# Kernel tuning notes

Measured on AMD Instinct MI355X. Metric: run time of the kernel, lower is better.

Reference implementation:

```python
import jax, jax.numpy as jnp
import numpy as np

B, T, D, H, O = 16384, 64, 64, 256, 1


def setup_inputs() -> dict:
    key = jax.random.key(0)
    ks = jax.random.split(key, 16)
    s = 0.05
    inp = {
        "x": jax.random.normal(ks[0], (B, T, D), dtype=jnp.float32),
        # RNNCell layer1: h1 = tanh(x @ W_ih1.T + b_ih1 + h1 @ W_hh1.T + b_hh1)
        "W_ih1": jax.random.normal(ks[1], (H, D), dtype=jnp.float32) * s,
        "b_ih1": jax.random.normal(ks[2], (H,), dtype=jnp.float32) * s,
        "W_hh1": jax.random.normal(ks[3], (H, H), dtype=jnp.float32) * s,
        "b_hh1": jax.random.normal(ks[4], (H,), dtype=jnp.float32) * s,
        # RNNCell layer2 (input is h1, size H)
        "W_ih2": jax.random.normal(ks[5], (H, H), dtype=jnp.float32) * s,
        "b_ih2": jax.random.normal(ks[6], (H,), dtype=jnp.float32) * s,
        "W_hh2": jax.random.normal(ks[7], (H, H), dtype=jnp.float32) * s,
        "b_hh2": jax.random.normal(ks[8], (H,), dtype=jnp.float32) * s,
        # output heads
        "W_o1": jax.random.normal(ks[9], (O, H), dtype=jnp.float32) * s,
        "b_o1": jax.random.normal(ks[10], (O,), dtype=jnp.float32) * s,
        "W_o2": jax.random.normal(ks[11], (O, H), dtype=jnp.float32) * s,
        "b_o2": jax.random.normal(ks[12], (O,), dtype=jnp.float32) * s,
        # gate: Linear(2H, H)
        "W_g": jax.random.normal(ks[13], (H, 2 * H), dtype=jnp.float32) * s,
        "b_g": jax.random.normal(ks[14], (H,), dtype=jnp.float32) * s,
    }
    return inp


def _gated_rnn(x, W_ih1, b_ih1, W_hh1, b_hh1, W_ih2, b_ih2, W_hh2, b_hh2,
               W_o1, b_o1, W_o2, b_o2, W_g, b_g):
    b = x.shape[0]
    h1_0 = jnp.zeros((b, H), dtype=x.dtype)
    h2_0 = jnp.zeros((b, H), dtype=x.dtype)
    u_0 = jnp.ones((b, H), dtype=x.dtype)

    # Precompute input projections for all timesteps: [T, B, H]
    x_proj = jnp.einsum('btd,hd->tbh', x, W_ih1) + b_ih1

    def step(carry, xp_t):
        h1, h2, u = carry
        h1 = jnp.tanh(xp_t + h1 @ W_hh1.T + b_hh1)
        z2 = jnp.tanh(h1 @ W_ih2.T + b_ih2 + h2 @ W_hh2.T + b_hh2)
        h2 = u * z2 + (1.0 - u) * h2
        out = jnp.tanh(h1 @ W_o1.T + b_o1) + jnp.tanh(h2 @ W_o2.T + b_o2)
        u = jax.nn.sigmoid(jnp.concatenate([h1, h2], axis=1) @ W_g.T + b_g)
        return (h1, h2, u), out

    _, outs = jax.lax.scan(step, (h1_0, h2_0, u_0), x_proj)  # outs: [T, B, O]
    outs = jnp.transpose(outs, (1, 0, 2))  # [B, T, O]
    if outs.shape[2] == 1:
        outs = outs[:, :, 0]  # mirror .squeeze(2)
    return outs


def reference(x, W_ih1, b_ih1, W_hh1, b_hh1, W_ih2, b_ih2, W_hh2, b_hh2,
              W_o1, b_o1, W_o2, b_o2, W_g, b_g):
    return _gated_rnn(x, W_ih1, b_ih1, W_hh1, b_hh1, W_ih2, b_ih2, W_hh2,
                      b_hh2, W_o1, b_o1, W_o2, b_o2, W_g, b_g)
```

## Files before the change

kernel.cpp:

```cpp
#include <hip/hip_runtime.h>
#include <hip/hip_bf16.h>

typedef __bf16 bf16_t;
typedef __bf16 bf16x8 __attribute__((ext_vector_type(8)));
typedef float f32x4 __attribute__((ext_vector_type(4)));
typedef int i32x4 __attribute__((ext_vector_type(4)));

#define HDIM 256
#define TSTEPS 64
#define DIN 64
#define BM 64
#define NBLK 256

__device__ __forceinline__ float fast_tanh(float x) {
    float e = __builtin_amdgcn_exp2f(x * 2.8853900817779268f);
    return 1.0f - 2.0f * __builtin_amdgcn_rcpf(e + 1.0f);
}
__device__ __forceinline__ float fast_sigmoid(float x) {
    float e = __builtin_amdgcn_exp2f(-x * 1.4426950408889634f);
    return __builtin_amdgcn_rcpf(1.0f + e);
}

__device__ __forceinline__ unsigned lds_addr(int row, int kb) {
    return (unsigned)(row * 512 + (kb ^ ((row & 7) << 4)));
}
__device__ __forceinline__ unsigned lx_addr(int row, int kb) {
    return (unsigned)(row * 128 + (kb ^ ((row & 7) << 4)));
}

__device__ __forceinline__ bf16x8 lds_ld8(const char* p) {
    return *(const bf16x8*)p;
}
__device__ __forceinline__ void lds_st1(char* p, bf16_t v) {
    *(bf16_t*)p = v;
}

#define BAR()                                                       \
    do {                                                            \
        __builtin_amdgcn_sched_barrier(0);                          \
        asm volatile("s_waitcnt lgkmcnt(0)\n\ts_barrier" ::: "memory"); \
        __builtin_amdgcn_sched_barrier(0);                          \
    } while (0)

__global__ void pack_w(const float* __restrict__ s0, const float* __restrict__ s1,
                       int ksplit, int stride0, int stride1, int off0, int off1,
                       int KC, bf16_t* __restrict__ dst) {
    int idx = blockIdx.x * 256 + threadIdx.x;
    int total = 256 * KC * 32;
    if (idx >= total) return;
    int i = idx & 7;
    int lane = (idx >> 3) & 63;
    int chunk = idx >> 9;
    int n2 = chunk & 1;
    int rest = chunk >> 1;
    int kc = rest % KC, wv = rest / KC;
    int nt = wv * 2 + n2;
    int n = nt * 16 + (lane & 15);
    int k = kc * 32 + ((lane >> 4) * 8) + i;
    float v = (k < ksplit) ? s0[n * stride0 + off0 + k]
                           : s1[n * stride1 + off1 + (k - ksplit)];
    dst[idx] = (bf16_t)v;
}

__global__ void pack_bias(const float* __restrict__ b_ih1, const float* __restrict__ b_hh1,
                          const float* __restrict__ b_ih2, const float* __restrict__ b_hh2,
                          const float* __restrict__ b_g,
                          float* __restrict__ bias1, float* __restrict__ bias2a,
                          float* __restrict__ biasg) {
    int j = threadIdx.x;
    bias1[j] = b_ih1[j] + b_hh1[j];
    bias2a[j] = b_ih2[j] + b_hh2[j];
    biasg[j] = b_g[j];
}

#define ISSUE(BUF, PB, N)                                            \
    _Pragma("unroll") for (int c = 0; c < (N); ++c)                  \
        BUF[c] = *(const bf16x8*)((PB) + c * 512 + (lane << 3));

#define GEMM_PH(NKK, BUF, ASRC, KC0, ACC)                                             \
    _Pragma("unroll") for (int kk = 0; kk < (NKK); ++kk) {                            \
        bf16x8 a_[4];                                                                 \
        _Pragma("unroll") for (int mt = 0; mt < 4; ++mt)                              \
            a_[mt] = lds_ld8((ASRC) + lds_addr(mt * 16 + l15,                         \
                                               ((KC0) + kk) * 64 + l4 * 16));         \
        _Pragma("unroll") for (int mt = 0; mt < 4; ++mt) {                            \
            ACC[mt][0] = __builtin_amdgcn_mfma_f32_16x16x32_bf16(a_[mt], BUF[kk * 2 + 0], ACC[mt][0], 0, 0, 0); \
            ACC[mt][1] = __builtin_amdgcn_mfma_f32_16x16x32_bf16(a_[mt], BUF[kk * 2 + 1], ACC[mt][1], 0, 0, 0); \
        }                                                                             \
    }

__global__ __launch_bounds__(512, 1) void rnn_main(
    const float* __restrict__ x,
    const bf16_t* __restrict__ pw_ih1,
    const bf16_t* __restrict__ pw_hh1,
    const bf16_t* __restrict__ pw_2a,
    const bf16_t* __restrict__ pw_2b,
    const bf16_t* __restrict__ pw_3,
    const float* __restrict__ bias1v, const float* __restrict__ bias2av,
    const float* __restrict__ biasgv,
    const float* __restrict__ wo1, const float* __restrict__ bo1p,
    const float* __restrict__ wo2, const float* __restrict__ bo2p,
    unsigned* __restrict__ gsync,
    float* __restrict__ out) {
    __shared__ char lds[90112];
    char* lh1 = lds;
    char* lh2 = lds + 32768;
    char* lx  = lds + 65536;
    float* lout = (float*)(lds + 73728);

    const int tid = threadIdx.x;
    const int wave = tid >> 6, lane = tid & 63;
    const int l15 = lane & 15, l4 = lane >> 4;
    const int b0 = blockIdx.x * BM;
    unsigned* gc = gsync + (blockIdx.x & 7) * 32;

    {
        i32x4 z = {0, 0, 0, 0};
        for (int i = tid; i < 4096; i += 512) ((i32x4*)lds)[i] = z;
    }

    f32x4 u_reg[4][2];
#pragma unroll
    for (int mt = 0; mt < 4; ++mt)
#pragma unroll
        for (int n2 = 0; n2 < 2; ++n2) u_reg[mt][n2] = (f32x4){1.f, 1.f, 1.f, 1.f};

    float bias1_r[2], bias2a_r[2], biasg_r[2];
#pragma unroll
    for (int n2 = 0; n2 < 2; ++n2) {
        int col = wave * 32 + n2 * 16 + l15;
        bias1_r[n2] = bias1v[col];
        bias2a_r[n2] = bias2av[col];
        biasg_r[n2] = biasgv[col];
    }
    const float bo1 = bo1p[0], bo2 = bo2p[0];
    const int orow = tid >> 3, oseg = tid & 7;
    const int xrow = tid >> 3, xc16 = (tid & 7) * 16;
    const float* xbase = x + (size_t)(b0 + xrow) * (TSTEPS * DIN) + (tid & 7) * 8;

    const bf16_t* base_ih1 = pw_ih1 + wave * 2048;
    const bf16_t* base_hh1 = pw_hh1 + wave * 8192;
    const bf16_t* base_2a  = pw_2a  + wave * 16384;
    const bf16_t* base_2b  = pw_2b  + wave * 8192;
    const bf16_t* base_3   = pw_3   + wave * 8192;

    bf16x8 R0[8], R1[8], R2[8];

    {
        f32x4 xv0 = __builtin_nontemporal_load((const f32x4*)xbase);
        f32x4 xv1 = __builtin_nontemporal_load((const f32x4*)(xbase + 4));
        bf16x8 xa;
        xa[0] = (bf16_t)xv0[0]; xa[1] = (bf16_t)xv0[1]; xa[2] = (bf16_t)xv0[2]; xa[3] = (bf16_t)xv0[3];
        xa[4] = (bf16_t)xv1[0]; xa[5] = (bf16_t)xv1[1]; xa[6] = (bf16_t)xv1[2]; xa[7] = (bf16_t)xv1[3];
        *(bf16x8*)(lx + lx_addr(xrow, xc16)) = xa;
    }
    ISSUE(R0, base_ih1, 4);
    ISSUE(R1, base_hh1, 8);
    ISSUE(R2, base_hh1 + 4096, 8);
    BAR();

    for (int t = 0; t < TSTEPS; ++t) {
        f32x4 acc[4][2];
#pragma unroll
        for (int mt = 0; mt < 4; ++mt)
#pragma unroll
            for (int n2 = 0; n2 < 2; ++n2) acc[mt][n2] = (f32x4){0.f, 0.f, 0.f, 0.f};
#pragma unroll
        for (int kk = 0; kk < 2; ++kk) {
            bf16x8 a_[4];
#pragma unroll
            for (int mt = 0; mt < 4; ++mt)
                a_[mt] = lds_ld8(lx + lx_addr(mt * 16 + l15, kk * 64 + l4 * 16));
#pragma unroll
            for (int mt = 0; mt < 4; ++mt) {
                acc[mt][0] = __builtin_amdgcn_mfma_f32_16x16x32_bf16(a_[mt], R0[kk * 2 + 0], acc[mt][0], 0, 0, 0);
                acc[mt][1] = __builtin_amdgcn_mfma_f32_16x16x32_bf16(a_[mt], R0[kk * 2 + 1], acc[mt][1], 0, 0, 0);
            }
        }
        ISSUE(R0, base_2a, 8);
        f32x4 xv0, xv1;
        {
            int tn = t + 1; if (tn > TSTEPS - 1) tn = TSTEPS - 1;
            const float* xp = xbase + tn * DIN;
            xv0 = __builtin_nontemporal_load((const f32x4*)xp);
            xv1 = __builtin_nontemporal_load((const f32x4*)(xp + 4));
        }
        GEMM_PH(4, R1, lh1, 0, acc)
        ISSUE(R1, base_2a + 4096, 8);
        GEMM_PH(4, R2, lh1, 4, acc)
        ISSUE(R2, base_2a + 8192, 8);

        float h1n[4][2][4];
#pragma unroll
        for (int mt = 0; mt < 4; ++mt)
#pragma unroll
            for (int n2 = 0; n2 < 2; ++n2)
#pragma unroll
                for (int r = 0; r < 4; ++r)
                    h1n[mt][n2][r] = fast_tanh(acc[mt][n2][r] + bias1_r[n2]);
        BAR();
#pragma unroll
        for (int mt = 0; mt < 4; ++mt)
#pragma unroll
            for (int n2 = 0; n2 < 2; ++n2)
#pragma unroll
                for (int r = 0; r < 4; ++r)
                    lds_st1(lh1 + lds_addr(mt * 16 + l4 * 4 + r,
                                           (wave * 32 + n2 * 16 + l15) * 2), (bf16_t)h1n[mt][n2][r]);
        BAR();

        f32x4 accz[4][2];
#pragma unroll
        for (int mt = 0; mt < 4; ++mt)
#pragma unroll
            for (int n2 = 0; n2 < 2; ++n2) accz[mt][n2] = (f32x4){0.f, 0.f, 0.f, 0.f};
        GEMM_PH(4, R0, lh1, 0, accz)
        ISSUE(R0, base_2a + 12288, 8);
        GEMM_PH(4, R1, lh1, 4, accz)
        ISSUE(R1, base_2b, 8);
        GEMM_PH(4, R2, lh2, 0, accz)
        ISSUE(R2, base_2b + 4096, 8);
        GEMM_PH(4, R0, lh2, 4, accz)
        ISSUE(R0, base_3, 8);

        float h2n[4][2][4];
#pragma unroll
        for (int mt = 0; mt < 4; ++mt)
#pragma unroll
            for (int n2 = 0; n2 < 2; ++n2)
#pragma unroll
                for (int r = 0; r < 4; ++r) {
                    float z2 = fast_tanh(accz[mt][n2][r] + bias2a_r[n2]);
                    float h2o = (float)*(const bf16_t*)(lh2 + lds_addr(mt * 16 + l4 * 4 + r,
                                                                       (wave * 32 + n2 * 16 + l15) * 2));
                    float un = u_reg[mt][n2][r];
                    h2n[mt][n2][r] = un * z2 + (1.f - un) * h2o;
                }
        BAR();
#pragma unroll
        for (int mt = 0; mt < 4; ++mt)
#pragma unroll
            for (int n2 = 0; n2 < 2; ++n2)
#pragma unroll
                for (int r = 0; r < 4; ++r)
                    lds_st1(lh2 + lds_addr(mt * 16 + l4 * 4 + r,
                                           (wave * 32 + n2 * 16 + l15) * 2), (bf16_t)h2n[mt][n2][r]);
        {
            bf16x8 xa;
            xa[0] = (bf16_t)xv0[0]; xa[1] = (bf16_t)xv0[1]; xa[2] = (bf16_t)xv0[2]; xa[3] = (bf16_t)xv0[3];
            xa[4] = (bf16_t)xv1[0]; xa[5] = (bf16_t)xv1[1]; xa[6] = (bf16_t)xv1[2]; xa[7] = (bf16_t)xv1[3];
            *(bf16x8*)(lx + lx_addr(xrow, xc16)) = xa;
        }

        f32x4 accg[4][2];
#pragma unroll
        for (int mt = 0; mt < 4; ++mt)
#pragma unroll
            for (int n2 = 0; n2 < 2; ++n2) accg[mt][n2] = (f32x4){0.f, 0.f, 0.f, 0.f};
        GEMM_PH(4, R1, lh1, 0, accg)
        ISSUE(R1, base_3 + 4096, 4);
        BAR();

        if (tid == 0)
            __hip_atomic_fetch_add(gc, 1u, __ATOMIC_RELAXED, __HIP_MEMORY_SCOPE_AGENT);

        GEMM_PH(4, R2, lh1, 4, accg)
        ISSUE(R2, base_3 + 6144, 4);
        GEMM_PH(4, R0, lh2, 0, accg)
        ISSUE(R0, base_ih1, 4);
        GEMM_PH(2, R1, lh2, 4, accg)
        ISSUE(R1, base_hh1, 8);
        GEMM_PH(2, R2, lh2, 6, accg)
        ISSUE(R2, base_hh1 + 4096, 8);

#pragma unroll
        for (int mt = 0; mt < 4; ++mt)
#pragma unroll
            for (int n2 = 0; n2 < 2; ++n2)
#pragma unroll
                for (int r = 0; r < 4; ++r)
                    u_reg[mt][n2][r] = fast_sigmoid(accg[mt][n2][r] + biasg_r[n2]);

        float s1 = 0.f, s2 = 0.f;
#pragma unroll
        for (int c = 0; c < 4; ++c) {
            int kb = oseg * 64 + c * 16;
            bf16x8 hv1 = lds_ld8(lh1 + lds_addr(orow, kb));
            bf16x8 hv2 = lds_ld8(lh2 + lds_addr(orow, kb));
            const float* w1p = wo1 + oseg * 32 + c * 8;
            const float* w2p = wo2 + oseg * 32 + c * 8;
            float4 w10 = *(const float4*)w1p, w11 = *(const float4*)(w1p + 4);
            float4 w20 = *(const float4*)w2p, w21 = *(const float4*)(w2p + 4);
            s1 += (float)hv1[0] * w10.x + (float)hv1[1] * w10.y + (float)hv1[2] * w10.z + (float)hv1[3] * w10.w;
            s1 += (float)hv1[4] * w11.x + (float)hv1[5] * w11.y + (float)hv1[6] * w11.z + (float)hv1[7] * w11.w;
            s2 += (float)hv2[0] * w20.x + (float)hv2[1] * w20.y + (float)hv2[2] * w20.z + (float)hv2[3] * w20.w;
            s2 += (float)hv2[4] * w21.x + (float)hv2[5] * w21.y + (float)hv2[6] * w21.z + (float)hv2[7] * w21.w;
        }
        s1 += __shfl_xor(s1, 1, 8); s1 += __shfl_xor(s1, 2, 8); s1 += __shfl_xor(s1, 4, 8);
        s2 += __shfl_xor(s2, 1, 8); s2 += __shfl_xor(s2, 2, 8); s2 += __shfl_xor(s2, 4, 8);
        if (oseg == 0)
            lout[orow * TSTEPS + t] = fast_tanh(s1 + bo1) + fast_tanh(s2 + bo2);

        if (tid == 0) {
            unsigned target = 32u * (unsigned)(t + 1);
            int guard = 0;
            while (__hip_atomic_load(gc, __ATOMIC_RELAXED, __HIP_MEMORY_SCOPE_AGENT) < target
                   && guard < 1500) {
                ++guard;
                __builtin_amdgcn_s_sleep(2);
            }
        }
        BAR();
    }

    {
        const float* lp = lout + tid * 8;
        f32x4 o0 = {lp[0], lp[1], lp[2], lp[3]};
        f32x4 o1 = {lp[4], lp[5], lp[6], lp[7]};
        float* op = out + (size_t)b0 * TSTEPS + tid * 8;
        *(f32x4*)op = o0;
        *(f32x4*)(op + 4) = o1;
    }
}

extern "C" void kernel_launch(void* const* d_in, const int* in_sizes, int n_in,
                              void* d_out, int out_size, void* d_ws, size_t ws_size,
                              hipStream_t stream) {
    const float* x = (const float*)d_in[0];
    const float* W_ih1 = (const float*)d_in[1];
    const float* b_ih1 = (const float*)d_in[2];
    const float* W_hh1 = (const float*)d_in[3];
    const float* b_hh1 = (const float*)d_in[4];
    const float* W_ih2 = (const float*)d_in[5];
    const float* b_ih2 = (const float*)d_in[6];
    const float* W_hh2 = (const float*)d_in[7];
    const float* b_hh2 = (const float*)d_in[8];
    const float* W_o1 = (const float*)d_in[9];
    const float* b_o1 = (const float*)d_in[10];
    const float* W_o2 = (const float*)d_in[11];
    const float* b_o2 = (const float*)d_in[12];
    const float* W_g = (const float*)d_in[13];
    const float* b_g = (const float*)d_in[14];

    char* ws = (char*)d_ws;
    bf16_t* pw_ih1 = (bf16_t*)(ws + 0);
    bf16_t* pw_hh1 = (bf16_t*)(ws + 32768);
    bf16_t* pw_2a = (bf16_t*)(ws + 163840);
    bf16_t* pw_2b = (bf16_t*)(ws + 425984);
    bf16_t* pw_3 = (bf16_t*)(ws + 557056);
    float* bias1 = (float*)(ws + 688128);
    float* bias2a = (float*)(ws + 689152);
    float* biasg = (float*)(ws + 690176);
    unsigned* gsync = (unsigned*)(ws + 692224);

    pack_w<<<32 * 2, 256, 0, stream>>>(W_ih1, W_ih1, 64, 64, 64, 0, 0, 2, pw_ih1);
    pack_w<<<32 * 8, 256, 0, stream>>>(W_hh1, W_hh1, 256, 256, 256, 0, 0, 8, pw_hh1);
    pack_w<<<32 * 16, 256, 0, stream>>>(W_ih2, W_hh2, 256, 256, 256, 0, 0, 16, pw_2a);
    pack_w<<<32 * 8, 256, 0, stream>>>(W_g, W_g, 256, 512, 512, 0, 0, 8, pw_2b);
    pack_w<<<32 * 8, 256, 0, stream>>>(W_g, W_g, 256, 512, 512, 256, 0, 8, pw_3);
    pack_bias<<<1, 256, 0, stream>>>(b_ih1, b_hh1, b_ih2, b_hh2, b_g, bias1, bias2a, biasg);
    hipMemsetAsync(gsync, 0, 1024, stream);

    rnn_main<<<NBLK, 512, 0, stream>>>(x, pw_ih1, pw_hh1, pw_2a, pw_2b, pw_3,
                                       bias1, bias2a, biasg, W_o1, b_o1, W_o2, b_o2,
                                       gsync, (float*)d_out);
}
```

Baseline: 1.990 ms.

## Double-buffer h1/h2 LDS state to drop write-after-read barriers

Gives the h1 and h2 hidden-state tiles ping-pong buffers in LDS, alternating by timestep parity. New values are written into the other buffer while the old one is still being read, which removes two of the per-step block barriers. It also moves one gate GEMM phase ahead of the remaining barrier. The cost is LDS growing from about 88KB to 152KB, and correctness now depends on the single remaining barrier per phase being enough for the swapped buffers.

Result: slower. 2.390 ms (+20.1%).

```diff
diff --git a/kernel.cpp b/kernel.cpp
--- a/kernel.cpp
+++ b/kernel.cpp
@@ -102,11 +102,9 @@
     const float* __restrict__ wo2, const float* __restrict__ bo2p,
     unsigned* __restrict__ gsync,
     float* __restrict__ out) {
-    __shared__ char lds[90112];
-    char* lh1 = lds;
-    char* lh2 = lds + 32768;
-    char* lx  = lds + 65536;
-    float* lout = (float*)(lds + 73728);
+    __shared__ char lds[155648];
+    char* lx = lds + 131072;
+    float* lout = (float*)(lds + 139264);
 
     const int tid = threadIdx.x;
     const int wave = tid >> 6, lane = tid & 63;
@@ -116,7 +114,7 @@
 
     {
         i32x4 z = {0, 0, 0, 0};
-        for (int i = tid; i < 4096; i += 512) ((i32x4*)lds)[i] = z;
+        for (int i = tid; i < 8192; i += 512) ((i32x4*)lds)[i] = z;
     }
 
     f32x4 u_reg[4][2];
@@ -160,6 +158,12 @@
     BAR();
 
     for (int t = 0; t < TSTEPS; ++t) {
+        const int p = t & 1;
+        char* Ar = lds + (p ? 32768 : 0);
+        char* Aw = lds + (p ? 0 : 32768);
+        char* Br = lds + 65536 + (p ? 32768 : 0);
+        char* Bw = lds + 65536 + (p ? 0 : 32768);
+
         f32x4 acc[4][2];
 #pragma unroll
         for (int mt = 0; mt < 4; ++mt)
@@ -185,45 +189,36 @@
             xv0 = __builtin_nontemporal_load((const f32x4*)xp);
             xv1 = __builtin_nontemporal_load((const f32x4*)(xp + 4));
         }
-        GEMM_PH(4, R1, lh1, 0, acc)
+        GEMM_PH(4, R1, Ar, 0, acc)
         ISSUE(R1, base_2a + 4096, 8);
-        GEMM_PH(4, R2, lh1, 4, acc)
+        GEMM_PH(4, R2, Ar, 4, acc)
         ISSUE(R2, base_2a + 8192, 8);
 
-        float h1n[4][2][4];
 #pragma unroll
         for (int mt = 0; mt < 4; ++mt)
 #pragma unroll
             for (int n2 = 0; n2 < 2; ++n2)
 #pragma unroll
                 for (int r = 0; r < 4; ++r)
-                    h1n[mt][n2][r] = fast_tanh(acc[mt][n2][r] + bias1_r[n2]);
+                    lds_st1(Aw + lds_addr(mt * 16 + l4 * 4 + r,
+                                          (wave * 32 + n2 * 16 + l15) * 2),
+                            (bf16_t)fast_tanh(acc[mt][n2][r] + bias1_r[n2]));
         BAR();
-#pragma unroll
-        for (int mt = 0; mt < 4; ++mt)
-#pragma unroll
-            for (int n2 = 0; n2 < 2; ++n2)
-#pragma unroll
-                for (int r = 0; r < 4; ++r)
-                    lds_st1(lh1 + lds_addr(mt * 16 + l4 * 4 + r,
-                                           (wave * 32 + n2 * 16 + l15) * 2), (bf16_t)h1n[mt][n2][r]);
-        BAR();
 
         f32x4 accz[4][2];
 #pragma unroll
         for (int mt = 0; mt < 4; ++mt)
 #pragma unroll
             for (int n2 = 0; n2 < 2; ++n2) accz[mt][n2] = (f32x4){0.f, 0.f, 0.f, 0.f};
-        GEMM_PH(4, R0, lh1, 0, accz)
+        GEMM_PH(4, R0, Aw, 0, accz)
         ISSUE(R0, base_2a + 12288, 8);
-        GEMM_PH(4, R1, lh1, 4, accz)
+        GEMM_PH(4, R1, Aw, 4, accz)
         ISSUE(R1, base_2b, 8);
-        GEMM_PH(4, R2, lh2, 0, accz)
+        GEMM_PH(4, R2, Br, 0, accz)
         ISSUE(R2, base_2b + 4096, 8);
-        GEMM_PH(4, R0, lh2, 4, accz)
+        GEMM_PH(4, R0, Br, 4, accz)
         ISSUE(R0, base_3, 8);
 
-        float h2n[4][2][4];
 #pragma unroll
         for (int mt = 0; mt < 4; ++mt)
 #pragma unroll
@@ -231,20 +226,13 @@
 #pragma unroll
                 for (int r = 0; r < 4; ++r) {
                     float z2 = fast_tanh(accz[mt][n2][r] + bias2a_r[n2]);
-                    float h2o = (float)*(const bf16_t*)(lh2 + lds_addr(mt * 16 + l4 * 4 + r,
-                                                                       (wave * 32 + n2 * 16 + l15) * 2));
+                    float h2o = (float)*(const bf16_t*)(Br + lds_addr(mt * 16 + l4 * 4 + r,
+                                                                      (wave * 32 + n2 * 16 + l15) * 2));
                     float un = u_reg[mt][n2][r];
-                    h2n[mt][n2][r] = un * z2 + (1.f - un) * h2o;
+                    lds_st1(Bw + lds_addr(mt * 16 + l4 * 4 + r,
+                                          (wave * 32 + n2 * 16 + l15) * 2),
+                            (bf16_t)(un * z2 + (1.f - un) * h2o));
                 }
-        BAR();
-#pragma unroll
-        for (int mt = 0; mt < 4; ++mt)
-#pragma unroll
-            for (int n2 = 0; n2 < 2; ++n2)
-#pragma unroll
-                for (int r = 0; r < 4; ++r)
-                    lds_st1(lh2 + lds_addr(mt * 16 + l4 * 4 + r,
-                                           (wave * 32 + n2 * 16 + l15) * 2), (bf16_t)h2n[mt][n2][r]);
         {
             bf16x8 xa;
             xa[0] = (bf16_t)xv0[0]; xa[1] = (bf16_t)xv0[1]; xa[2] = (bf16_t)xv0[2]; xa[3] = (bf16_t)xv0[3];
@@ -257,20 +245,20 @@
         for (int mt = 0; mt < 4; ++mt)
 #pragma unroll
             for (int n2 = 0; n2 < 2; ++n2) accg[mt][n2] = (f32x4){0.f, 0.f, 0.f, 0.f};
-        GEMM_PH(4, R1, lh1, 0, accg)
+        GEMM_PH(4, R1, Aw, 0, accg)
         ISSUE(R1, base_3 + 4096, 4);
+        GEMM_PH(4, R2, Aw, 4, accg)
+        ISSUE(R2, base_3 + 6144, 4);
         BAR();
 
         if (tid == 0)
             __hip_atomic_fetch_add(gc, 1u, __ATOMIC_RELAXED, __HIP_MEMORY_SCOPE_AGENT);
 
-        GEMM_PH(4, R2, lh1, 4, accg)
-        ISSUE(R2, base_3 + 6144, 4);
-        GEMM_PH(4, R0, lh2, 0, accg)
+        GEMM_PH(4, R0, Bw, 0, accg)
         ISSUE(R0, base_ih1, 4);
-        GEMM_PH(2, R1, lh2, 4, accg)
+        GEMM_PH(2, R1, Bw, 4, accg)
         ISSUE(R1, base_hh1, 8);
-        GEMM_PH(2, R2, lh2, 6, accg)
+        GEMM_PH(2, R2, Bw, 6, accg)
         ISSUE(R2, base_hh1 + 4096, 8);
 
 #pragma unroll
@@ -285,8 +273,8 @@
 #pragma unroll
         for (int c = 0; c < 4; ++c) {
             int kb = oseg * 64 + c * 16;
-            bf16x8 hv1 = lds_ld8(lh1 + lds_addr(orow, kb));
-            bf16x8 hv2 = lds_ld8(lh2 + lds_addr(orow, kb));
+            bf16x8 hv1 = lds_ld8(Aw + lds_addr(orow, kb));
+            bf16x8 hv2 = lds_ld8(Bw + lds_addr(orow, kb));
             const float* w1p = wo1 + oseg * 32 + c * 8;
             const float* w2p = wo2 + oseg * 32 + c * 8;
             float4 w10 = *(const float4*)w1p, w11 = *(const float4*)(w1p + 4);
```
